# Kernel tuning notes

Hardware: AMD Instinct MI355X
Metric: run time of the kernel (lower is better)

Reference implementation:

```python
import jax, jax.numpy as jnp
import numpy as np

K = 30  # kNN neighbors (DynamicEdgeConvParams default)

def _knn_idx(x, k):
    # x: [B,N,C] -> indices of k nearest neighbors in feature space, [B,N,k]
    x2 = jnp.sum(x * x, axis=-1)                      # [B,N]
    d = x2[:, :, None] + x2[:, None, :] - 2.0 * jnp.einsum('bnc,bmc->bnm', x, x)
    _, idx = jax.lax.top_k(-d, k)                     # includes self (dist 0)
    return idx

def _edge_conv(x, w0, b0, w1, b1, k):
    # DynamicEdgeConv: kNN on x, edge feat [x_i, x_j - x_i], MLP, max-aggr
    idx = _knn_idx(x, k)                              # [B,N,k]
    xj = jax.vmap(lambda xb, ib: xb[ib])(x, idx)      # [B,N,k,C] gather
    xi = jnp.broadcast_to(x[:, :, None, :], xj.shape)
    e = jnp.concatenate([xi, xj - xi], axis=-1)       # [B,N,k,2C]
    h = jax.nn.relu(jnp.einsum('bnkc,cd->bnkd', e, w0) + b0)
    h = jnp.einsum('bnkc,cd->bnkd', h, w1) + b1
    return jnp.max(h, axis=2)                         # [B,N,out]

def setup_inputs() -> dict:
    key = jax.random.key(0)
    ks = jax.random.split(key, 16)
    def w(k, shape):
        fan_in = shape[0]
        return jax.random.normal(k, shape, jnp.float32) / np.sqrt(fan_in)
    B, N = 16, 2048
    return {
        'pos': jax.random.normal(ks[0], (B, N, 3), jnp.float32),
        'c1_w0': w(ks[1], (6, 64)),   'c1_b0': jnp.zeros((64,), jnp.float32),
        'c1_w1': w(ks[2], (64, 64)),  'c1_b1': jnp.zeros((64,), jnp.float32),
        'c2_w0': w(ks[3], (128, 64)), 'c2_b0': jnp.zeros((64,), jnp.float32),
        'c2_w1': w(ks[4], (64, 64)),  'c2_b1': jnp.zeros((64,), jnp.float32),
        'c3_w0': w(ks[5], (128, 64)), 'c3_b0': jnp.zeros((64,), jnp.float32),
        'c3_w1': w(ks[6], (64, 64)),  'c3_b1': jnp.zeros((64,), jnp.float32),
        'mlp_w0': w(ks[7], (192, 1024)), 'mlp_b0': jnp.zeros((1024,), jnp.float32),
        'mlp_w1': w(ks[8], (1024, 256)), 'mlp_b1': jnp.zeros((256,), jnp.float32),
        'mlp_w2': w(ks[9], (256, 128)),  'mlp_b2': jnp.zeros((128,), jnp.float32),
        'fin_w': w(ks[10], (128, 3)),    'fin_b': jnp.zeros((3,), jnp.float32),
    }

def reference(pos, c1_w0, c1_b0, c1_w1, c1_b1, c2_w0, c2_b0, c2_w1, c2_b1,
              c3_w0, c3_b0, c3_w1, c3_b1, mlp_w0, mlp_b0, mlp_w1, mlp_b1,
              mlp_w2, mlp_b2, fin_w, fin_b):
    x1 = _edge_conv(pos, c1_w0, c1_b0, c1_w1, c1_b1, K)   # [B,N,64]
    x2 = _edge_conv(x1, c2_w0, c2_b0, c2_w1, c2_b1, K)    # [B,N,64]
    x3 = _edge_conv(x2, c3_w0, c3_b0, c3_w1, c3_b1, K)    # [B,N,64]
    h = jnp.concatenate([x1, x2, x3], axis=-1)            # [B,N,192]
    h = jax.nn.relu(h @ mlp_w0 + mlp_b0)
    h = jax.nn.relu(h @ mlp_w1 + mlp_b1)
    h = h @ mlp_w2 + mlp_b2                               # [B,N,128]
    return h @ fin_w + fin_b                              # [B,N,3]
```

## Files before the change

kernel.cpp:

```cpp
#include <hip/hip_runtime.h>
#include <hip/hip_bf16.h>
#include <cfloat>
#include <cstddef>

#define BB 16
#define NN 2048
#define KNN 30
#define MC 8192

using bf16 = __hip_bfloat16;
typedef short short8 __attribute__((ext_vector_type(8)));
typedef float floatx4 __attribute__((ext_vector_type(4)));

constexpr size_t XT_O  = 0;
constexpr size_t NRM_O = XT_O  + (size_t)BB*64*NN;
constexpr size_t A_O   = NRM_O + (size_t)BB*NN;
constexpr size_t U_O   = A_O   + (size_t)BB*NN*64;
constexpr size_t H_O   = U_O   + (size_t)BB*NN*64;
constexpr size_t WS_F  = H_O   + (size_t)BB*NN*192;
constexpr size_t H1C_S = 0;
constexpr size_t H2C_S = 8388608;
constexpr size_t WB_S  = 11534336;
constexpr size_t WB1_S = WB_S + 0;
constexpr size_t WB2_S = WB_S + 196608;
constexpr size_t WB3_S = WB_S + 458752;

__device__ __attribute__((aligned(16))) float g_ws[WS_F];
__device__ int   g_idx[(size_t)BB*NN*KNN];
__device__ int   g_isbf16;

__device__ __forceinline__ float b2f(bf16 x){ return __bfloat162float(x); }
__device__ __forceinline__ float ldi(const void* p, size_t i){
  return g_isbf16 ? b2f(((const bf16*)p)[i]) : ((const float*)p)[i];
}
__device__ __forceinline__ short f2bs(float v){
  bf16 h = __float2bfloat16(v);
  return *reinterpret_cast<short*>(&h);
}
__device__ __forceinline__ float bs2f(short s){
  bf16 h = *reinterpret_cast<bf16*>(&s);
  return __bfloat162float(h);
}
__device__ __forceinline__ unsigned fmono(float x){
  unsigned u = __float_as_uint(x);
  return ((int)u < 0) ? ~u : (u | 0x80000000u);
}

__global__ __launch_bounds__(256) void k_sniff(const unsigned* __restrict__ posw){
  __shared__ int cnt[256];
  const int tid = threadIdx.x;
  int c = 0;
  for(int k=0;k<8;k++){
    unsigned w = posw[tid*8+k];
    unsigned code = (w & 0x7F80u) >> 7;
    if(code >= 119u && code <= 129u) c++;
  }
  cnt[tid] = c; __syncthreads();
  for(int s=128;s>0;s>>=1){ if(tid<s) cnt[tid]+=cnt[tid+s]; __syncthreads(); }
  if(tid==0) g_isbf16 = (cnt[0] > 1024) ? 1 : 0;
}

__global__ __launch_bounds__(256) void k_diag(bf16* __restrict__ out, int n, float v){
  int t = blockIdx.x*256 + threadIdx.x;
  if(t < n) out[t] = __float2bfloat16(v);
}

__global__ __launch_bounds__(256) void k_prep(const void* __restrict__ pos){
  int t = blockIdx.x*256 + threadIdx.x;
  int b = t >> 11, i = t & (NN-1);
  float x = ldi(pos, (size_t)t*3+0), y = ldi(pos, (size_t)t*3+1), z = ldi(pos, (size_t)t*3+2);
  float* Xb = g_ws + XT_O + (size_t)b*64*NN;
  Xb[0*NN+i] = x; Xb[1*NN+i] = y; Xb[2*NN+i] = z;
  g_ws[NRM_O + t] = x*x + y*y + z*z;
}

template<int C>
__global__ __launch_bounds__(512, 4) void k_knn(){
  const int tid  = threadIdx.x;
  const int wid  = tid >> 6, lane = tid & 63;
  const int b    = blockIdx.x >> 8;
  const int i0   = (blockIdx.x & 255) * 8;
  const size_t gi0 = (size_t)b*NN + i0;
  __shared__ unsigned dlds[4][NN];
  const float* Xb  = g_ws + XT_O + (size_t)b*64*NN;
  const float* nrm = g_ws + NRM_O;

  const int j0 = tid*4;
  float4 nj4 = *(const float4*)&nrm[(size_t)b*NN + j0];

  float acc[8][4];
  #pragma unroll
  for(int r=0;r<8;r++)
    #pragma unroll
    for(int s=0;s<4;s++) acc[r][s] = 0.f;

  constexpr int CH  = (C == 3) ? 3 : 2;
  constexpr int NCH = C / CH;
  float4 vb[2][CH];
  #pragma unroll
  for(int cc=0; cc<CH; cc++) vb[0][cc] = *(const float4*)&Xb[(size_t)cc*NN + j0];
  #pragma unroll
  for(int k=0; k<NCH; k++){
    if(k+1 < NCH){
      #pragma unroll
      for(int cc=0; cc<CH; cc++)
        vb[(k+1)&1][cc] = *(const float4*)&Xb[(size_t)((k+1)*CH+cc)*NN + j0];
    }
    #pragma unroll
    for(int cc=0; cc<CH; cc++){
      const int c = k*CH + cc;
      const float4 vj = vb[k&1][cc];
      const float* xr = &Xb[(size_t)c*NN + i0];
      #pragma unroll
      for(int r=0;r<8;r++){
        float xc = xr[r];
        acc[r][0] = fmaf(xc, vj.x, acc[r][0]);
        acc[r][1] = fmaf(xc, vj.y, acc[r][1]);
        acc[r][2] = fmaf(xc, vj.z, acc[r][2]);
        acc[r][3] = fmaf(xc, vj.w, acc[r][3]);
      }
    }
  }

  #pragma unroll
  for(int r=0;r<4;r++){
    float nIr = nrm[gi0 + r];
    uint4 kv;
    kv.x = fmono(fmaf(-2.f, acc[r][0], nIr + nj4.x));
    kv.y = fmono(fmaf(-2.f, acc[r][1], nIr + nj4.y));
    kv.z = fmono(fmaf(-2.f, acc[r][2], nIr + nj4.z));
    kv.w = fmono(fmaf(-2.f, acc[r][3], nIr + nj4.w));
    *(uint4*)&dlds[r][j0] = kv;
  }
  __syncthreads();
  unsigned kk[32];
  if(wid < 4){
    const unsigned* drow = dlds[wid];
    #pragma unroll
    for(int q=0;q<32;q++) kk[q] = drow[lane + (q<<6)];
  }
  __syncthreads();
  #pragma unroll
  for(int r=4;r<8;r++){
    float nIr = nrm[gi0 + r];
    uint4 kv;
    kv.x = fmono(fmaf(-2.f, acc[r][0], nIr + nj4.x));
    kv.y = fmono(fmaf(-2.f, acc[r][1], nIr + nj4.y));
    kv.z = fmono(fmaf(-2.f, acc[r][2], nIr + nj4.z));
    kv.w = fmono(fmaf(-2.f, acc[r][3], nIr + nj4.w));
    *(uint4*)&dlds[r-4][j0] = kv;
  }
  __syncthreads();
  if(wid >= 4){
    const unsigned* drow = dlds[wid-4];
    #pragma unroll
    for(int q=0;q<32;q++) kk[q] = drow[lane + (q<<6)];
  }

  const size_t rowbase = (gi0 + wid)*KNN;

  unsigned lo = 0x80000000u, hi = 0xFFFFFFFFu;
  unsigned T = 0; bool exact = false;
  while(hi - lo > 1u){
    unsigned mid = lo + ((hi - lo) >> 1);
    int tot = 0;
    #pragma unroll
    for(int q=0;q<32;q++) tot += (int)__popcll(__ballot(kk[q] < mid));
    if(tot == KNN){ T = mid; exact = true; break; }
    if(tot < KNN) lo = mid; else hi = mid;
  }

  int base = 0;
  if(exact){
    #pragma unroll
    for(int q=0;q<32;q++){
      bool p = kk[q] < T;
      unsigned long long m = __ballot(p);
      if(p){
        int pos = base + __builtin_amdgcn_mbcnt_hi((unsigned)(m>>32),
                        __builtin_amdgcn_mbcnt_lo((unsigned)m, 0u));
        g_idx[rowbase + pos] = lane + (q<<6);
      }
      base += (int)__popcll(m);
    }
  } else {
    #pragma unroll
    for(int q=0;q<32;q++){
      bool p = kk[q] < lo;
      unsigned long long m = __ballot(p);
      if(p){
        int pos = base + __builtin_amdgcn_mbcnt_hi((unsigned)(m>>32),
                        __builtin_amdgcn_mbcnt_lo((unsigned)m, 0u));
        g_idx[rowbase + pos] = lane + (q<<6);
      }
      base += (int)__popcll(m);
    }
    #pragma unroll
    for(int q=0;q<32;q++){
      bool p = kk[q] == lo;
      unsigned long long m = __ballot(p);
      if(p){
        int pos = base + __builtin_amdgcn_mbcnt_hi((unsigned)(m>>32),
                        __builtin_amdgcn_mbcnt_lo((unsigned)m, 0u));
        if(pos < KNN) g_idx[rowbase + pos] = lane + (q<<6);
      }
      base += (int)__popcll(m);
    }
  }
}

template<int C, bool EXTIN>
__global__ __launch_bounds__(256) void k_stage_pre(const void* __restrict__ Xin, int xOff,
    int rowStride, int colOff, const void* __restrict__ W0, const void* __restrict__ b0){
  __shared__ float Wd[C*64];
  __shared__ float Wb[C*64];
  __shared__ float bb[64];
  __shared__ float xs[4][C];
  const int tid = threadIdx.x;
  for(int t=tid; t<C*64; t+=256){
    float top = ldi(W0, t), bot = ldi(W0, (size_t)C*64 + t);
    Wd[t] = top - bot; Wb[t] = bot;
  }
  if(tid < 64) bb[tid] = ldi(b0, tid);
  const int wid = tid >> 6, lane = tid & 63;
  const int point = blockIdx.x*4 + wid;
  if(lane < C){
    float x;
    if(EXTIN) x = ldi(Xin, (size_t)point*rowStride + colOff + lane);
    else      x = g_ws[(size_t)xOff + (size_t)point*rowStride + colOff + lane];
    xs[wid][lane] = x;
  }
  __syncthreads();
  float a = bb[lane], u = 0.f;
  for(int c=0;c<C;c++){
    float xc = xs[wid][c];
    a = fmaf(xc, Wd[c*64 + lane], a);
    u = fmaf(xc, Wb[c*64 + lane], u);
  }
  g_ws[A_O + (size_t)point*64 + lane] = a;
  g_ws[U_O + (size_t)point*64 + lane] = u;
}

template<bool WRITE_NEXT>
__global__ __launch_bounds__(256) void k_edge_agg(const void* __restrict__ W1,
    const void* __restrict__ b1, int colOff){
  __shared__ short hk_hi[4][32][64] __attribute__((aligned(16)));
  __shared__ short hk_lo[4][32][64] __attribute__((aligned(16)));
  const int tid = threadIdx.x;
  const int wid = tid >> 6, lane = tid & 63;
  const int ml = lane & 15, kgl = lane >> 4;
  short8 wh[2][4], wl[2][4];
  #pragma unroll
  for(int kt=0; kt<2; kt++)
    #pragma unroll
    for(int nt=0; nt<4; nt++)
      #pragma unroll
      for(int j=0; j<8; j++){
        float w = ldi(W1, (size_t)(kt*32 + kgl*8 + j)*64 + nt*16 + ml);
        short hi = f2bs(w);
        wh[kt][nt][j] = hi;
        wl[kt][nt][j] = f2bs(w - bs2f(hi));
      }
  const float bias = ldi(b1, lane);
  hk_hi[wid][30][lane] = 0; hk_hi[wid][31][lane] = 0;
  hk_lo[wid][30][lane] = 0; hk_lo[wid][31][lane] = 0;
  for(int pp=0; pp<4; pp++){
    const int point = blockIdx.x*16 + wid*4 + pp;
    const int b = point >> 11, i = point & (NN-1);
    const float a = g_ws[A_O + (size_t)point*64 + lane];
    const int* ip = g_idx + (size_t)point*KNN;
    const float* Ub = g_ws + U_O + (size_t)b*NN*64;
    int jv = 0;
    if(lane < KNN) jv = ip[lane] & (NN-1);
    #pragma unroll
    for(int kk=0; kk<KNN; kk++){
      int j = __shfl(jv, kk, 64);
      float h = fmaxf(a + Ub[(size_t)j*64 + lane], 0.f);
      short hi = f2bs(h);
      hk_hi[wid][kk][lane] = hi;
      hk_lo[wid][kk][lane] = f2bs(h - bs2f(hi));
    }
    floatx4 acc[2][4];
    #pragma unroll
    for(int t=0;t<2;t++)
      #pragma unroll
      for(int nt=0;nt<4;nt++) acc[t][nt] = (floatx4){0.f,0.f,0.f,0.f};
    #pragma unroll
    for(int t=0;t<2;t++){
      #pragma unroll
      for(int kt=0;kt<2;kt++){
        short8 ah = *(const short8*)&hk_hi[wid][t*16+ml][kt*32 + kgl*8];
        short8 al = *(const short8*)&hk_lo[wid][t*16+ml][kt*32 + kgl*8];
        #pragma unroll
        for(int nt=0;nt<4;nt++){
          acc[t][nt] = __builtin_amdgcn_mfma_f32_16x16x32_bf16(ah, wh[kt][nt], acc[t][nt], 0,0,0);
          acc[t][nt] = __builtin_amdgcn_mfma_f32_16x16x32_bf16(ah, wl[kt][nt], acc[t][nt], 0,0,0);
          acc[t][nt] = __builtin_amdgcn_mfma_f32_16x16x32_bf16(al, wh[kt][nt], acc[t][nt], 0,0,0);
        }
      }
    }
    float cmax[4];
    #pragma unroll
    for(int nt=0;nt<4;nt++){
      float mx = -FLT_MAX;
      #pragma unroll
      for(int t=0;t<2;t++)
        #pragma unroll
        for(int reg=0;reg<4;reg++){
          int m = t*16 + kgl*4 + reg;
          if(m < KNN) mx = fmaxf(mx, acc[t][nt][reg]);
        }
      mx = fmaxf(mx, __shfl_xor(mx, 16, 64));
      mx = fmaxf(mx, __shfl_xor(mx, 32, 64));
      cmax[nt] = mx;
    }
    float r01 = (lane & 16) ? cmax[1] : cmax[0];
    float r23 = (lane & 16) ? cmax[3] : cmax[2];
    float accf = ((lane & 32) ? r23 : r01) + bias;
    g_ws[H_O + (size_t)point*192 + colOff + lane] = accf;
    if(WRITE_NEXT){
      g_ws[XT_O + ((size_t)b*64 + lane)*NN + i] = accf;
      float sq = accf*accf;
      #pragma unroll
      for(int off=32; off>0; off>>=1) sq += __shfl_xor(sq, off, 64);
      if(lane == 0) g_ws[NRM_O + point] = sq;
    }
  }
}

__global__ __launch_bounds__(256) void k_wconv3(const void* __restrict__ W0,
    const void* __restrict__ W1, const void* __restrict__ W2){
  int t = blockIdx.x*256 + threadIdx.x;
  const void* W; int dstOff, rel, lg;
  if(t < 196608)      { W = W0; dstOff = (int)WB1_S; rel = t;          lg = 10; }
  else if(t < 458752) { W = W1; dstOff = (int)WB2_S; rel = t - 196608; lg = 8;  }
  else                { W = W2; dstOff = (int)WB3_S; rel = t - 458752; lg = 7;  }
  int k = rel >> lg, n = rel & ((1<<lg)-1);
  short* dst = (short*)g_ws + dstOff;
  dst[((size_t)((k>>3) << lg) + ((size_t)n))*8 + (k&7)] = f2bs(ldi(W, rel));
}

template<bool ABF16, bool RELU, bool OUTBF16>
__global__ __launch_bounds__(256) void k_mgemm(int aOff, int wOffS, const void* __restrict__ bias,
    int outOff, int Kd, int Nn){
  __shared__ short As[4*128*8] __attribute__((aligned(16)));
  __shared__ short Bs[4*128*8] __attribute__((aligned(16)));
  const int tid = threadIdx.x;
  const int lane = tid & 63, wid = tid >> 6;
  const int waveM = wid >> 1, waveN = wid & 1;
  const int m0 = blockIdx.x * 128, n0 = blockIdx.y * 128;
  const int sm = tid >> 1, skg0 = (tid & 1) * 2;
  const int bn = tid & 127, bkg = tid >> 7;
  const short* Wb = (const short*)g_ws + wOffS;
  floatx4 acc[4][4];
  #pragma unroll
  for(int a=0;a<4;a++)
    #pragma unroll
    for(int bq=0;bq<4;bq++) acc[a][bq] = (floatx4){0.f,0.f,0.f,0.f};

  for(int k0 = 0; k0 < Kd; k0 += 32){
    if(ABF16){
      const short* Ab = (const short*)g_ws + aOff + (size_t)(m0+sm)*Kd + k0 + skg0*8;
      short8 v0 = *(const short8*)Ab;
      short8 v1 = *(const short8*)(Ab+8);
      *(short8*)&As[((skg0  )*128 + sm)*8] = v0;
      *(short8*)&As[((skg0+1)*128 + sm)*8] = v1;
    } else {
      const float* Af = g_ws + aOff + (size_t)(m0+sm)*Kd + k0 + skg0*8;
      float4 f0 = *(const float4*)(Af+0);
      float4 f1 = *(const float4*)(Af+4);
      float4 f2 = *(const float4*)(Af+8);
      float4 f3 = *(const float4*)(Af+12);
      short8 s0, s1;
      s0[0]=f2bs(f0.x); s0[1]=f2bs(f0.y); s0[2]=f2bs(f0.z); s0[3]=f2bs(f0.w);
      s0[4]=f2bs(f1.x); s0[5]=f2bs(f1.y); s0[6]=f2bs(f1.z); s0[7]=f2bs(f1.w);
      s1[0]=f2bs(f2.x); s1[1]=f2bs(f2.y); s1[2]=f2bs(f2.z); s1[3]=f2bs(f2.w);
      s1[4]=f2bs(f3.x); s1[5]=f2bs(f3.y); s1[6]=f2bs(f3.z); s1[7]=f2bs(f3.w);
      *(short8*)&As[((skg0  )*128 + sm)*8] = s0;
      *(short8*)&As[((skg0+1)*128 + sm)*8] = s1;
    }
    #pragma unroll
    for(int i=0;i<2;i++){
      int kg = bkg + i*2;
      const short* src = Wb + ((size_t)((k0>>3) + kg)*Nn + n0 + bn)*8;
      *(short8*)&Bs[(kg*128 + bn)*8] = *(const short8*)src;
    }
    __syncthreads();
    const int kgl = lane >> 4, ml = lane & 15;
    short8 af[4], bf[4];
    #pragma unroll
    for(int t=0;t<4;t++){
      af[t] = *(const short8*)&As[(kgl*128 + waveM*64 + t*16 + ml)*8];
      bf[t] = *(const short8*)&Bs[(kgl*128 + waveN*64 + t*16 + ml)*8];
    }
    #pragma unroll
    for(int tm=0;tm<4;tm++)
      #pragma unroll
      for(int tn=0;tn<4;tn++)
        acc[tm][tn] = __builtin_amdgcn_mfma_f32_16x16x32_bf16(af[tm], bf[tn], acc[tm][tn], 0, 0, 0);
    __syncthreads();
  }
  const int kgl = lane >> 4, ml = lane & 15;
  #pragma unroll
  for(int tn=0;tn<4;tn++){
    int n = n0 + waveN*64 + tn*16 + ml;
    float bv = ldi(bias, n);
    #pragma unroll
    for(int tm=0;tm<4;tm++){
      #pragma unroll
      for(int reg=0;reg<4;reg++){
        int m = m0 + waveM*64 + tm*16 + kgl*4 + reg;
        float v = acc[tm][tn][reg] + bv;
        if(RELU) v = fmaxf(v, 0.f);
        if(OUTBF16) ((short*)g_ws)[(size_t)outOff + (size_t)m*Nn + n] = f2bs(v);
        else        g_ws[(size_t)outOff + (size_t)m*Nn + n] = v;
      }
    }
  }
}

__global__ __launch_bounds__(256) void k_mgemm_fin(int aOff, int wOffS,
    const void* __restrict__ bias, const void* __restrict__ FW, const void* __restrict__ FB,
    void* __restrict__ out, int outPointBase){
  __shared__ short As[4*128*8] __attribute__((aligned(16)));
  __shared__ short Bs[4*128*8] __attribute__((aligned(16)));
  __shared__ float h3[128][129];
  __shared__ float wf[384];
  __shared__ float fb3[3];
  const int Kd = 256, Nn = 128;
  const int tid = threadIdx.x;
  const int lane = tid & 63, wid = tid >> 6;
  const int waveM = wid >> 1, waveN = wid & 1;
  const int m0 = blockIdx.x * 128;
  const int sm = tid >> 1, skg0 = (tid & 1) * 2;
  const int bn = tid & 127, bkg = tid >> 7;
  const short* Wb = (const short*)g_ws + wOffS;
  for(int t=tid; t<384; t+=256) wf[t] = ldi(FW, t);
  if(tid < 3) fb3[tid] = ldi(FB, tid);
  floatx4 acc[4][4];
  #pragma unroll
  for(int a=0;a<4;a++)
    #pragma unroll
    for(int bq=0;bq<4;bq++) acc[a][bq] = (floatx4){0.f,0.f,0.f,0.f};

  for(int k0 = 0; k0 < Kd; k0 += 32){
    const short* Ab = (const short*)g_ws + aOff + (size_t)(m0+sm)*Kd + k0 + skg0*8;
    short8 v0 = *(const short8*)Ab;
    short8 v1 = *(const short8*)(Ab+8);
    *(short8*)&As[((skg0  )*128 + sm)*8] = v0;
    *(short8*)&As[((skg0+1)*128 + sm)*8] = v1;
    #pragma unroll
    for(int i=0;i<2;i++){
      int kg = bkg + i*2;
      const short* src = Wb + ((size_t)((k0>>3) + kg)*Nn + bn)*8;
      *(short8*)&Bs[(kg*128 + bn)*8] = *(const short8*)src;
    }
    __syncthreads();
    const int kgl = lane >> 4, ml = lane & 15;
    short8 af[4], bf[4];
    #pragma unroll
    for(int t=0;t<4;t++){
      af[t] = *(const short8*)&As[(kgl*128 + waveM*64 + t*16 + ml)*8];
      bf[t] = *(const short8*)&Bs[(kgl*128 + waveN*64 + t*16 + ml)*8];
    }
    #pragma unroll
    for(int tm=0;tm<4;tm++)
      #pragma unroll
      for(int tn=0;tn<4;tn++)
        acc[tm][tn] = __builtin_amdgcn_mfma_f32_16x16x32_bf16(af[tm], bf[tn], acc[tm][tn], 0, 0, 0);
    __syncthreads();
  }
  const int kgl = lane >> 4, ml = lane & 15;
  #pragma unroll
  for(int tn=0;tn<4;tn++){
    int n = waveN*64 + tn*16 + ml;
    float bv = ldi(bias, n);
    #pragma unroll
    for(int tm=0;tm<4;tm++){
      #pragma unroll
      for(int reg=0;reg<4;reg++){
        int m = waveM*64 + tm*16 + kgl*4 + reg;
        h3[m][n] = acc[tm][tn][reg] + bv;
      }
    }
  }
  __syncthreads();
  if(tid < 128){
    float a0 = fb3[0], a1 = fb3[1], a2 = fb3[2];
    #pragma unroll 8
    for(int c=0;c<128;c++){
      float x = h3[tid][c];
      a0 = fmaf(x, wf[c*3+0], a0);
      a1 = fmaf(x, wf[c*3+1], a1);
      a2 = fmaf(x, wf[c*3+2], a2);
    }
    size_t o = (size_t)(outPointBase + blockIdx.x*128 + tid)*3;
    if(g_isbf16){
      bf16* ob = (bf16*)out;
      ob[o+0] = __float2bfloat16(a0); ob[o+1] = __float2bfloat16(a1); ob[o+2] = __float2bfloat16(a2);
    } else {
      float* of = (float*)out;
      of[o+0] = a0; of[o+1] = a1; of[o+2] = a2;
    }
  }
}

extern "C" void kernel_launch(void* const* d_in, const int* in_sizes, int n_in,
                              void* d_out, int out_size, void* d_ws, size_t ws_size,
                              hipStream_t stream){
  (void)d_ws; (void)ws_size;
  static const int EXP[21] = {98304, 384,64, 4096,64, 8192,64, 4096,64, 8192,64, 4096,64,
                              196608,1024, 262144,256, 32768,128, 384,3};
  const void* in[21];
  int posmatch = 0;
  bool run = false;
  if(n_in == 21){
    for(int e=0; e<21; e++) posmatch += (in_sizes[e] == EXP[e]) ? 1 : 0;
    if(posmatch == 21){
      for(int e=0; e<21; e++) in[e] = d_in[e];
      run = true;
    } else {
      bool used[21] = {false}; const void* m[21]; bool ok = true;
      for(int e=0; e<21 && ok; e++){
        int hit = -1;
        for(int i2=0; i2<21; i2++)
          if(!used[i2] && in_sizes[i2] == EXP[e]){ hit = i2; break; }
        if(hit < 0) ok = false;
        else { used[hit] = true; m[e] = d_in[hit]; }
      }
      if(ok){ for(int e=0; e<21; e++) in[e] = m[e]; run = true; }
    }
  }
  if(!run){
    float V = 1000.f*(float)n_in + 10.f*(float)posmatch;
    k_diag<<<(out_size+255)/256, 256, 0, stream>>>((bf16*)d_out, out_size, V);
    return;
  }
  const void* pos  = in[0];
  const void* c1w0 = in[1];  const void* c1b0 = in[2];
  const void* c1w1 = in[3];  const void* c1b1 = in[4];
  const void* c2w0 = in[5];  const void* c2b0 = in[6];
  const void* c2w1 = in[7];  const void* c2b1 = in[8];
  const void* c3w0 = in[9];  const void* c3b0 = in[10];
  const void* c3w1 = in[11]; const void* c3b1 = in[12];
  const void* mw0  = in[13]; const void* mb0  = in[14];
  const void* mw1  = in[15]; const void* mb1  = in[16];
  const void* mw2  = in[17]; const void* mb2  = in[18];
  const void* fw   = in[19]; const void* fb   = in[20];

  dim3 b256(256);
  dim3 b512(512);
  k_sniff<<<1, b256, 0, stream>>>((const unsigned*)pos);
  k_prep<<<128, b256, 0, stream>>>(pos);

  k_knn<3><<<4096, b512, 0, stream>>>();
  k_stage_pre<3,true><<<8192, b256, 0, stream>>>(pos, 0, 3, 0, c1w0, c1b0);
  k_edge_agg<true><<<2048, b256, 0, stream>>>(c1w1, c1b1, 0);

  k_knn<64><<<4096, b512, 0, stream>>>();
  k_stage_pre<64,false><<<8192, b256, 0, stream>>>(nullptr, (int)H_O, 192, 0, c2w0, c2b0);
  k_edge_agg<true><<<2048, b256, 0, stream>>>(c2w1, c2b1, 64);

  k_knn<64><<<4096, b512, 0, stream>>>();
  k_stage_pre<64,false><<<8192, b256, 0, stream>>>(nullptr, (int)H_O, 192, 64, c3w0, c3b0);
  k_edge_agg<false><<<2048, b256, 0, stream>>>(c3w1, c3b1, 128);

  k_wconv3<<<1920, b256, 0, stream>>>(mw0, mw1, mw2);

  for(int ch=0; ch<4; ch++){
    int ainOff = (int)(H_O + (size_t)ch*MC*192);
    k_mgemm<false,true ,true ><<<dim3(64,8), b256, 0, stream>>>(ainOff,     (int)WB1_S, mb0, (int)H1C_S, 192, 1024);
    k_mgemm<true ,true ,true ><<<dim3(64,2), b256, 0, stream>>>((int)H1C_S, (int)WB2_S, mb1, (int)H2C_S, 1024, 256);
    k_mgemm_fin<<<64, b256, 0, stream>>>((int)H2C_S, (int)WB3_S, mb2, fw, fb, d_out, ch*MC);
  }
}
```

Measured before the change: 1.080 ms.

## Tighten kNN bisection bounds, widen distance channel chunks, amortize stage_pre weight loads

New measurement: 1.092 ms. Within noise of the previous version (+1.2%).

```diff
diff --git a/kernel.cpp b/kernel.cpp
--- a/kernel.cpp
+++ b/kernel.cpp
@@ -94,7 +94,7 @@
     #pragma unroll
     for(int s=0;s<4;s++) acc[r][s] = 0.f;
 
-  constexpr int CH  = (C == 3) ? 3 : 2;
+  constexpr int CH  = (C == 3) ? 3 : 4;
   constexpr int NCH = C / CH;
   float4 vb[2][CH];
   #pragma unroll
@@ -159,7 +159,22 @@
 
   const size_t rowbase = (gi0 + wid)*KNN;
 
-  unsigned lo = 0x80000000u, hi = 0xFFFFFFFFu;
+  unsigned mn = 0xFFFFFFFFu, mx = 0u;
+  #pragma unroll
+  for(int q=0;q<32;q++){
+    unsigned kq = kk[q];
+    mn = kq < mn ? kq : mn;
+    mx = kq > mx ? kq : mx;
+  }
+  #pragma unroll
+  for(int off=32; off>0; off>>=1){
+    unsigned mno = (unsigned)__shfl_xor((int)mn, off, 64);
+    unsigned mxo = (unsigned)__shfl_xor((int)mx, off, 64);
+    mn = mno < mn ? mno : mn;
+    mx = mxo > mx ? mxo : mx;
+  }
+  unsigned lo = mn, hi = mx + 1u;
+
   unsigned T = 0; bool exact = false;
   while(hi - lo > 1u){
     unsigned mid = lo + ((hi - lo) >> 1);
@@ -215,30 +230,34 @@
   __shared__ float Wd[C*64];
   __shared__ float Wb[C*64];
   __shared__ float bb[64];
-  __shared__ float xs[4][C];
+  __shared__ float xs[16][C];
   const int tid = threadIdx.x;
   for(int t=tid; t<C*64; t+=256){
     float top = ldi(W0, t), bot = ldi(W0, (size_t)C*64 + t);
     Wd[t] = top - bot; Wb[t] = bot;
   }
   if(tid < 64) bb[tid] = ldi(b0, tid);
+  const int pbase = blockIdx.x*16;
+  for(int t=tid; t<16*C; t+=256){
+    int p = t / C, c = t - p*C;
+    float x;
+    if(EXTIN) x = ldi(Xin, (size_t)(pbase+p)*rowStride + colOff + c);
+    else      x = g_ws[(size_t)xOff + (size_t)(pbase+p)*rowStride + colOff + c];
+    xs[p][c] = x;
+  }
+  __syncthreads();
   const int wid = tid >> 6, lane = tid & 63;
-  const int point = blockIdx.x*4 + wid;
-  if(lane < C){
-    float x;
-    if(EXTIN) x = ldi(Xin, (size_t)point*rowStride + colOff + lane);
-    else      x = g_ws[(size_t)xOff + (size_t)point*rowStride + colOff + lane];
-    xs[wid][lane] = x;
-  }
-  __syncthreads();
-  float a = bb[lane], u = 0.f;
-  for(int c=0;c<C;c++){
-    float xc = xs[wid][c];
-    a = fmaf(xc, Wd[c*64 + lane], a);
-    u = fmaf(xc, Wb[c*64 + lane], u);
-  }
-  g_ws[A_O + (size_t)point*64 + lane] = a;
-  g_ws[U_O + (size_t)point*64 + lane] = u;
+  for(int pp=0; pp<4; pp++){
+    const int point = pbase + wid*4 + pp;
+    float a = bb[lane], u = 0.f;
+    for(int c=0;c<C;c++){
+      float xc = xs[wid*4+pp][c];
+      a = fmaf(xc, Wd[c*64 + lane], a);
+      u = fmaf(xc, Wb[c*64 + lane], u);
+    }
+    g_ws[A_O + (size_t)point*64 + lane] = a;
+    g_ws[U_O + (size_t)point*64 + lane] = u;
+  }
 }
 
 template<bool WRITE_NEXT>
@@ -554,15 +573,15 @@
   k_prep<<<128, b256, 0, stream>>>(pos);
 
   k_knn<3><<<4096, b512, 0, stream>>>();
-  k_stage_pre<3,true><<<8192, b256, 0, stream>>>(pos, 0, 3, 0, c1w0, c1b0);
+  k_stage_pre<3,true><<<2048, b256, 0, stream>>>(pos, 0, 3, 0, c1w0, c1b0);
   k_edge_agg<true><<<2048, b256, 0, stream>>>(c1w1, c1b1, 0);
 
   k_knn<64><<<4096, b512, 0, stream>>>();
-  k_stage_pre<64,false><<<8192, b256, 0, stream>>>(nullptr, (int)H_O, 192, 0, c2w0, c2b0);
+  k_stage_pre<64,false><<<2048, b256, 0, stream>>>(nullptr, (int)H_O, 192, 0, c2w0, c2b0);
   k_edge_agg<true><<<2048, b256, 0, stream>>>(c2w1, c2b1, 64);
 
   k_knn<64><<<4096, b512, 0, stream>>>();
-  k_stage_pre<64,false><<<8192, b256, 0, stream>>>(nullptr, (int)H_O, 192, 64, c3w0, c3b0);
+  k_stage_pre<64,false><<<2048, b256, 0, stream>>>(nullptr, (int)H_O, 192, 64, c3w0, c3b0);
   k_edge_agg<false><<<2048, b256, 0, stream>>>(c3w1, c3b1, 128);
 
   k_wconv3<<<1920, b256, 0, stream>>>(mw0, mw1, mw2);
```
